# Performance work log

Hardware: AMD Instinct MI355X
Metric: run time of the kernel (lower is better)

The kernel has to match this reference:

```python
import jax, jax.numpy as jnp
import numpy as np

B, N, E = 4, 10000, 160000
IN, OUT, H, ED = 64, 128, 2, 1
SLOPE = 0.2  # GATv2Conv default negative_slope


def _seg_softmax(logits, seg, n):
    # logits: [Ef, H]; softmax over edges sharing the same dst node, per head
    m = jax.ops.segment_max(logits, seg, num_segments=n)
    e = jnp.exp(logits - m[seg])
    d = jax.ops.segment_sum(e, seg, num_segments=n)
    return e / d[seg]


def setup_inputs() -> dict:
    key = jax.random.key(0)
    ks = jax.random.split(key, 10)
    s = 0.05
    return {
        "node_feats": jax.random.normal(ks[0], (B, N, IN), jnp.float32),
        "edge_index": jax.random.randint(ks[1], (2, E), 0, N, dtype=jnp.int64),
        "edge_attr": jax.random.normal(ks[2], (E, ED), jnp.float32),
        "Wl": jax.random.normal(ks[3], (IN, H * OUT), jnp.float32) * s,
        "bl": jax.random.normal(ks[4], (H * OUT,), jnp.float32) * s,
        "Wr": jax.random.normal(ks[5], (IN, H * OUT), jnp.float32) * s,
        "br": jax.random.normal(ks[6], (H * OUT,), jnp.float32) * s,
        "We": jax.random.normal(ks[7], (ED, H * OUT), jnp.float32) * s,
        "att": jax.random.normal(ks[8], (H, OUT), jnp.float32) * s,
        "bias": jax.random.normal(ks[9], (H * OUT,), jnp.float32) * s,
    }


def reference(node_feats, edge_index, edge_attr, Wl, bl, Wr, br, We, att, bias):
    src, dst = edge_index[0], edge_index[1]
    # PyG add_self_loops(fill_value='mean'): self-loop attr = mean of incoming edge attrs per node
    ones = jnp.ones((E,), edge_attr.dtype)
    deg = jax.ops.segment_sum(ones, dst, num_segments=N)
    loop_attr = jax.ops.segment_sum(edge_attr, dst, num_segments=N) / jnp.maximum(deg, 1.0)[:, None]
    sl = jnp.arange(N)
    src_f = jnp.concatenate([src, sl])           # [Ef] with Ef = E + N
    dst_f = jnp.concatenate([dst, sl])
    e_feat = (jnp.concatenate([edge_attr, loop_attr], axis=0) @ We).reshape(-1, H, OUT)  # [Ef,H,C]

    xl = (node_feats @ Wl + bl).reshape(B, N, H, OUT)  # lin_l(x)
    xr = (node_feats @ Wr + br).reshape(B, N, H, OUT)  # lin_r(x)

    # GATv2: score on leaky_relu(x_l[src] + x_r[dst] + lin_edge(e))
    msg = jax.nn.leaky_relu(xl[:, src_f] + xr[:, dst_f] + e_feat[None], SLOPE)  # [B,Ef,H,C]
    logits = jnp.einsum('behc,hc->beh', msg, att)                               # [B,Ef,H]
    alpha = jax.vmap(lambda l: _seg_softmax(l, dst_f, N))(logits)               # [B,Ef,H]

    weighted = alpha[..., None] * xl[:, src_f]                                  # [B,Ef,H,C]
    out = jax.vmap(lambda w: jax.ops.segment_sum(w, dst_f, num_segments=N))(weighted)  # [B,N,H,C]
    return out.reshape(B, N, H * OUT) + bias
```

## Files before the change

kernel.cpp:

```cpp
#include <hip/hip_runtime.h>
#include <hip/hip_bf16.h>

#define BQ 4
#define NN 10000
#define EE 160000
#define HC 256
#define SLOPEK 0.2f
#define CAPE 128

typedef __attribute__((ext_vector_type(8))) short bf16x8;
typedef __attribute__((ext_vector_type(4))) float f32x4;
typedef __attribute__((ext_vector_type(2))) float f32x2;

__device__ __forceinline__ unsigned short f2bf(float f) {
    unsigned int u = __float_as_uint(f);
    u = (u + 0x7FFFu + ((u >> 16) & 1u)) >> 16;
    return (unsigned short)u;
}
__device__ __forceinline__ f32x2 bf2(unsigned int u) {
    return (f32x2){__uint_as_float(u << 16), __uint_as_float(u & 0xFFFF0000u)};
}

__global__ __launch_bounds__(256) void k_wpack(
    const float* __restrict__ Wl, const float* __restrict__ bl,
    const float* __restrict__ Wr, const float* __restrict__ br,
    unsigned short* __restrict__ wp, float* __restrict__ bp,
    int* __restrict__ zbase)
{
    if (blockIdx.x >= 130) {
        const int i = (blockIdx.x - 130) * 256 + threadIdx.x;
        if (i < 2 * NN) zbase[i] = 0;
        return;
    }
    const int tid = blockIdx.x * 256 + threadIdx.x;
    if (tid < 32768) {
        const int j  = tid & 7;
        const int l  = (tid >> 3) & 63;
        const int s  = (tid >> 9) & 1;
        const int ct = tid >> 10;
        const int col = ct * 16 + (l & 15);
        const int kk  = s * 32 + ((l >> 4) << 3) + j;
        const float w = (col < 256) ? Wl[kk * 256 + col] : Wr[kk * 256 + (col - 256)];
        wp[tid] = f2bf(w);
    } else if (tid < 32768 + 512) {
        const int c = tid - 32768;
        bp[c] = (c < 256) ? bl[c] : br[c - 256];
    }
}

__global__ __launch_bounds__(256) void k_pre(
    const float* __restrict__ x, const unsigned short* __restrict__ wp,
    const float* __restrict__ bp,
    unsigned short* __restrict__ xl, unsigned short* __restrict__ xr,
    const int* __restrict__ ei, const float* __restrict__ ea,
    int* __restrict__ cnt, float* __restrict__ asum,
    int2* __restrict__ cmeta)
{
    if (blockIdx.x >= 625) {
        const int e = (blockIdx.x - 625) * 256 + threadIdx.x;
        const int   sn = ei[e];
        const int   d  = ei[EE + e];
        const float a  = ea[e];
        const int pos  = atomicAdd(&cnt[d], 1);
        atomicAdd(&asum[d], a);
        if (pos < CAPE - 1)
            cmeta[d * CAPE + pos] = make_int2(sn << 10, __float_as_int(a));
        return;
    }
    const int w = threadIdx.x >> 6, l = threadIdx.x & 63;
    const int row0 = blockIdx.x * 64 + w * 16;
    const int arow = row0 + (l & 15);
    const float* xp = x + (size_t)arow * 64 + ((l >> 4) << 3);

    bf16x8 a[2];
#pragma unroll
    for (int s = 0; s < 2; ++s) {
        const float4 lo = *reinterpret_cast<const float4*>(xp + s * 32);
        const float4 hi = *reinterpret_cast<const float4*>(xp + s * 32 + 4);
        union { bf16x8 v; unsigned short u[8]; } t;
        t.u[0] = f2bf(lo.x); t.u[1] = f2bf(lo.y); t.u[2] = f2bf(lo.z); t.u[3] = f2bf(lo.w);
        t.u[4] = f2bf(hi.x); t.u[5] = f2bf(hi.y); t.u[6] = f2bf(hi.z); t.u[7] = f2bf(hi.w);
        a[s] = t.v;
    }
    const int colb = l & 15;
    const int rsub = (l >> 4) << 2;

    for (int g = 0; g < 8; ++g) {
        f32x4 acc[4] = {{0.f,0.f,0.f,0.f},{0.f,0.f,0.f,0.f},
                        {0.f,0.f,0.f,0.f},{0.f,0.f,0.f,0.f}};
#pragma unroll
        for (int c = 0; c < 4; ++c) {
            const int ct = g * 4 + c;
            const bf16x8 b0 = *reinterpret_cast<const bf16x8*>(wp + (((ct * 2 + 0) * 64 + l) << 3));
            const bf16x8 b1 = *reinterpret_cast<const bf16x8*>(wp + (((ct * 2 + 1) * 64 + l) << 3));
            acc[c] = __builtin_amdgcn_mfma_f32_16x16x32_bf16(a[0], b0, acc[c], 0, 0, 0);
            acc[c] = __builtin_amdgcn_mfma_f32_16x16x32_bf16(a[1], b1, acc[c], 0, 0, 0);
        }
#pragma unroll
        for (int c = 0; c < 4; ++c) {
            const int col = (g * 4 + c) * 16 + colb;
            const float bv = bp[col];
#pragma unroll
            for (int r = 0; r < 4; ++r) {
                const int row = row0 + rsub + r;
                const int bb = (row >= 20000) ? (row >= 30000 ? 3 : 2)
                                              : (row >= 10000 ? 1 : 0);
                const int n = row - bb * NN;
                const unsigned short h = f2bf(acc[c][r] + bv);
                if (col < 256) xl[(((size_t)(n * 4 + bb)) << 8) + col] = h;
                else           xr[(((size_t)(n * 4 + bb)) << 8) + (col - 256)] = h;
            }
        }
    }
}

__global__ __launch_bounds__(256) void k_gat(
    const unsigned short* __restrict__ xl, const unsigned short* __restrict__ xr,
    const int* __restrict__ cnt, const float* __restrict__ asum,
    const int2* __restrict__ cmeta,
    const float* __restrict__ We, const float* __restrict__ att,
    const float* __restrict__ bias, float* __restrict__ outp)
{
    const int t  = threadIdx.x;
    const int wv = t >> 6, ln = t & 63;
    const int W  = blockIdx.x * 4 + wv;
    const int n  = W >> 1;
    const int bp = W & 1;
    const int b  = bp * 2 + (ln >> 5);
    const int ch0 = (ln & 31) * 8;

    int dg0 = cnt[n];
    if (dg0 > 63) dg0 = 63;
    const int dg = __builtin_amdgcn_readfirstlane(dg0);
    const int2 md0 = cmeta[n * CAPE + ln];
    int   ms = md0.x;
    float ma = __int_as_float(md0.y);
    if (ln == dg) {
        ms = n << 10;
        ma = asum[n] / fmaxf((float)dg, 1.0f);
    }
    const int ntot = dg + 1;

    f32x2 we2[4], at2[4], xr2[4], acc2[4];
    {
        const float4* Wp = reinterpret_cast<const float4*>(We + ch0);
        const float4* Ap = reinterpret_cast<const float4*>(att + ch0);
#pragma unroll
        for (int j = 0; j < 2; ++j) {
            const float4 w4 = Wp[j], a4 = Ap[j];
            we2[2*j+0] = (f32x2){w4.x, w4.y};
            we2[2*j+1] = (f32x2){w4.z, w4.w};
            at2[2*j+0] = (f32x2){a4.x, a4.y};
            at2[2*j+1] = (f32x2){a4.z, a4.w};
        }
        const uint4 r0 = *reinterpret_cast<const uint4*>(
            xr + ((size_t)n << 10) + (b << 8) + ch0);
        xr2[0] = bf2(r0.x); xr2[1] = bf2(r0.y); xr2[2] = bf2(r0.z); xr2[3] = bf2(r0.w);
    }
    const f32x2 km1 = {SLOPEK - 1.f, SLOPEK - 1.f};
    const f32x2 z2  = {0.f, 0.f};
#pragma unroll
    for (int k = 0; k < 4; ++k) acc2[k] = z2;
    float sh = 0.f;

    const unsigned short* __restrict__ xlp = xl + (b << 8) + ch0;

    uint4 A0, A1, A2, A3;
    float ea0, ea1, ea2, ea3;

#define LOADSLOT(S, IDX) do { \
        const int ii_ = (IDX); \
        const int ic_ = ii_ < dg ? ii_ : dg; \
        const int   s_ = __builtin_amdgcn_readlane(ms, ic_); \
        ea##S = __int_as_float(__builtin_amdgcn_readlane(__float_as_int(ma), ic_)); \
        A##S = *reinterpret_cast<const uint4*>(xlp + s_); \
    } while (0)

    auto edgeC = [&](const uint4& A, float a0) {
        f32x2 xv2[4];
        xv2[0] = bf2(A.x); xv2[1] = bf2(A.y); xv2[2] = bf2(A.z); xv2[3] = bf2(A.w);

        const f32x2 a02 = {a0, a0};
        f32x2 qa = z2, qb = z2;
#pragma unroll
        for (int j = 0; j < 4; ++j) {
            f32x2 s = xv2[j] + xr2[j];
            f32x2 v = __builtin_elementwise_fma(a02, we2[j], s);
            f32x2 vm = __builtin_elementwise_min(v, z2);
            v = __builtin_elementwise_fma(km1, vm, v);
            if (j & 1) qb = __builtin_elementwise_fma(v, at2[j], qb);
            else       qa = __builtin_elementwise_fma(v, at2[j], qa);
        }
        const f32x2 q2 = qa + qb;
        float p = q2.x + q2.y;
        p += __shfl_xor(p, 1);
        p += __shfl_xor(p, 2);
        p += __shfl_xor(p, 4);
        p += __shfl_xor(p, 8);
        const float e = __expf(p);
        sh += e;
        const f32x2 e2 = {e, e};
#pragma unroll
        for (int j = 0; j < 4; ++j)
            acc2[j] = __builtin_elementwise_fma(e2, xv2[j], acc2[j]);
    };

    LOADSLOT(0, 0);
    LOADSLOT(1, 1);
    LOADSLOT(2, 2);

    int i = 0;
    for (; i + 3 < ntot; i += 4) {
        LOADSLOT(3, i + 3); edgeC(A0, ea0);
        LOADSLOT(0, i + 4); edgeC(A1, ea1);
        LOADSLOT(1, i + 5); edgeC(A2, ea2);
        LOADSLOT(2, i + 6); edgeC(A3, ea3);
    }
    if (i     < ntot) edgeC(A0, ea0);
    if (i + 1 < ntot) edgeC(A1, ea1);
    if (i + 2 < ntot) edgeC(A2, ea2);
#undef LOADSLOT

    const float inv = 1.0f / sh;
    float* ob = outp + (((size_t)(b * NN + n)) << 8) + ch0;
    const float4* Bp = reinterpret_cast<const float4*>(bias + ch0);
#pragma unroll
    for (int j = 0; j < 2; ++j) {
        const float4 b4 = Bp[j];
        float4 o;
        o.x = fmaf(acc2[2*j+0].x, inv, b4.x);
        o.y = fmaf(acc2[2*j+0].y, inv, b4.y);
        o.z = fmaf(acc2[2*j+1].x, inv, b4.z);
        o.w = fmaf(acc2[2*j+1].y, inv, b4.w);
        reinterpret_cast<float4*>(ob)[j] = o;
    }
}

extern "C" void kernel_launch(void* const* d_in, const int* in_sizes, int n_in,
                              void* d_out, int out_size, void* d_ws, size_t ws_size,
                              hipStream_t stream)
{
    (void)in_sizes; (void)n_in; (void)out_size; (void)ws_size;
    const float* x    = (const float*)d_in[0];
    const int*   ei   = (const int*)d_in[1];
    const float* ea   = (const float*)d_in[2];
    const float* Wl   = (const float*)d_in[3];
    const float* bl   = (const float*)d_in[4];
    const float* Wr   = (const float*)d_in[5];
    const float* br   = (const float*)d_in[6];
    const float* We   = (const float*)d_in[7];
    const float* att  = (const float*)d_in[8];
    const float* bias = (const float*)d_in[9];
    float* outp = (float*)d_out;

    const size_t R = (size_t)BQ * NN;
    unsigned short* xl16 = (unsigned short*)d_ws;
    unsigned short* xr16 = xl16 + R * HC;
    int*   cnt   = (int*)(xr16 + R * HC);
    float* asum  = (float*)(cnt + NN);
    int2*  cmeta = (int2*)(asum + NN);
    unsigned short* wp = (unsigned short*)(cmeta + (size_t)NN * CAPE);
    float* bp    = (float*)(wp + 32768);

    k_wpack<<<130 + (2 * NN + 255) / 256, 256, 0, stream>>>(Wl, bl, Wr, br, wp, bp, cnt);
    k_pre  <<<1250, 256, 0, stream>>>(x, wp, bp, xl16, xr16,
                                      ei, ea, cnt, asum, cmeta);
    k_gat  <<<(2 * NN) / 4, 256, 0, stream>>>(xl16, xr16, cnt, asum, cmeta,
                                              We, att, bias, outp);
}
```

Before: 89.98 us.

## Stage projection outputs in LDS for coalesced stores; deepen gather prefetch to 8

The projection kernel now writes bf16 results into a shared-memory tile and then emits 16-byte coalesced row stores to xl/xr, replacing scattered 2-byte global stores. The gather loop in the attention kernel is widened from a 4-deep to an 8-deep rotating prefetch of neighbor rows, to hide more memory latency. The exchange is extra LDS use and two barriers per half in k_pre, plus more registers in k_gat, which may reduce occupancy.

```diff
diff --git a/kernel.cpp b/kernel.cpp
--- a/kernel.cpp
+++ b/kernel.cpp
@@ -56,6 +56,8 @@
     int* __restrict__ cnt, float* __restrict__ asum,
     int2* __restrict__ cmeta)
 {
+    __shared__ unsigned short st[64][264];
+
     if (blockIdx.x >= 625) {
         const int e = (blockIdx.x - 625) * 256 + threadIdx.x;
         const int   sn = ei[e];
@@ -67,7 +69,8 @@
             cmeta[d * CAPE + pos] = make_int2(sn << 10, __float_as_int(a));
         return;
     }
-    const int w = threadIdx.x >> 6, l = threadIdx.x & 63;
+    const int t = threadIdx.x;
+    const int w = t >> 6, l = t & 63;
     const int row0 = blockIdx.x * 64 + w * 16;
     const int arow = row0 + (l & 15);
     const float* xp = x + (size_t)arow * 64 + ((l >> 4) << 3);
@@ -77,40 +80,45 @@
     for (int s = 0; s < 2; ++s) {
         const float4 lo = *reinterpret_cast<const float4*>(xp + s * 32);
         const float4 hi = *reinterpret_cast<const float4*>(xp + s * 32 + 4);
-        union { bf16x8 v; unsigned short u[8]; } t;
-        t.u[0] = f2bf(lo.x); t.u[1] = f2bf(lo.y); t.u[2] = f2bf(lo.z); t.u[3] = f2bf(lo.w);
-        t.u[4] = f2bf(hi.x); t.u[5] = f2bf(hi.y); t.u[6] = f2bf(hi.z); t.u[7] = f2bf(hi.w);
-        a[s] = t.v;
+        union { bf16x8 v; unsigned short u[8]; } tt;
+        tt.u[0] = f2bf(lo.x); tt.u[1] = f2bf(lo.y); tt.u[2] = f2bf(lo.z); tt.u[3] = f2bf(lo.w);
+        tt.u[4] = f2bf(hi.x); tt.u[5] = f2bf(hi.y); tt.u[6] = f2bf(hi.z); tt.u[7] = f2bf(hi.w);
+        a[s] = tt.v;
     }
     const int colb = l & 15;
     const int rsub = (l >> 4) << 2;
 
-    for (int g = 0; g < 8; ++g) {
-        f32x4 acc[4] = {{0.f,0.f,0.f,0.f},{0.f,0.f,0.f,0.f},
-                        {0.f,0.f,0.f,0.f},{0.f,0.f,0.f,0.f}};
-#pragma unroll
-        for (int c = 0; c < 4; ++c) {
-            const int ct = g * 4 + c;
-            const bf16x8 b0 = *reinterpret_cast<const bf16x8*>(wp + (((ct * 2 + 0) * 64 + l) << 3));
-            const bf16x8 b1 = *reinterpret_cast<const bf16x8*>(wp + (((ct * 2 + 1) * 64 + l) << 3));
-            acc[c] = __builtin_amdgcn_mfma_f32_16x16x32_bf16(a[0], b0, acc[c], 0, 0, 0);
-            acc[c] = __builtin_amdgcn_mfma_f32_16x16x32_bf16(a[1], b1, acc[c], 0, 0, 0);
-        }
-#pragma unroll
-        for (int c = 0; c < 4; ++c) {
-            const int col = (g * 4 + c) * 16 + colb;
-            const float bv = bp[col];
-#pragma unroll
-            for (int r = 0; r < 4; ++r) {
-                const int row = row0 + rsub + r;
-                const int bb = (row >= 20000) ? (row >= 30000 ? 3 : 2)
-                                              : (row >= 10000 ? 1 : 0);
-                const int n = row - bb * NN;
-                const unsigned short h = f2bf(acc[c][r] + bv);
-                if (col < 256) xl[(((size_t)(n * 4 + bb)) << 8) + col] = h;
-                else           xr[(((size_t)(n * 4 + bb)) << 8) + (col - 256)] = h;
+    for (int h = 0; h < 2; ++h) {
+        for (int g4 = 0; g4 < 4; ++g4) {
+            f32x4 acc[4] = {{0.f,0.f,0.f,0.f},{0.f,0.f,0.f,0.f},
+                            {0.f,0.f,0.f,0.f},{0.f,0.f,0.f,0.f}};
+#pragma unroll
+            for (int c = 0; c < 4; ++c) {
+                const int ct = h * 16 + g4 * 4 + c;
+                const bf16x8 b0 = *reinterpret_cast<const bf16x8*>(wp + (((ct * 2 + 0) * 64 + l) << 3));
+                const bf16x8 b1 = *reinterpret_cast<const bf16x8*>(wp + (((ct * 2 + 1) * 64 + l) << 3));
+                acc[c] = __builtin_amdgcn_mfma_f32_16x16x32_bf16(a[0], b0, acc[c], 0, 0, 0);
+                acc[c] = __builtin_amdgcn_mfma_f32_16x16x32_bf16(a[1], b1, acc[c], 0, 0, 0);
             }
-        }
+#pragma unroll
+            for (int c = 0; c < 4; ++c) {
+                const int colh = (g4 * 4 + c) * 16 + colb;
+                const float bv = bp[h * 256 + colh];
+#pragma unroll
+                for (int r = 0; r < 4; ++r)
+                    st[w * 16 + rsub + r][colh] = f2bf(acc[c][r] + bv);
+            }
+        }
+        __syncthreads();
+        unsigned short* __restrict__ dstb = h ? xr : xl;
+        for (int rr = (t >> 5); rr < 64; rr += 8) {
+            const int row = blockIdx.x * 64 + rr;
+            const int bb = row / NN;
+            const int n = row - bb * NN;
+            const uint4 v = *reinterpret_cast<const uint4*>(&st[rr][(t & 31) * 8]);
+            *reinterpret_cast<uint4*>(dstb + (((size_t)(n * 4 + bb)) << 8) + (t & 31) * 8) = v;
+        }
+        __syncthreads();
     }
 }
 
@@ -165,8 +173,8 @@
 
     const unsigned short* __restrict__ xlp = xl + (b << 8) + ch0;
 
-    uint4 A0, A1, A2, A3;
-    float ea0, ea1, ea2, ea3;
+    uint4 A0, A1, A2, A3, A4, A5, A6, A7;
+    float ea0, ea1, ea2, ea3, ea4, ea5, ea6, ea7;
 
 #define LOADSLOT(S, IDX) do { \
         const int ii_ = (IDX); \
@@ -205,20 +213,27 @@
             acc2[j] = __builtin_elementwise_fma(e2, xv2[j], acc2[j]);
     };
 
-    LOADSLOT(0, 0);
-    LOADSLOT(1, 1);
-    LOADSLOT(2, 2);
+    LOADSLOT(0, 0); LOADSLOT(1, 1); LOADSLOT(2, 2); LOADSLOT(3, 3);
+    LOADSLOT(4, 4); LOADSLOT(5, 5); LOADSLOT(6, 6);
 
     int i = 0;
-    for (; i + 3 < ntot; i += 4) {
-        LOADSLOT(3, i + 3); edgeC(A0, ea0);
-        LOADSLOT(0, i + 4); edgeC(A1, ea1);
-        LOADSLOT(1, i + 5); edgeC(A2, ea2);
-        LOADSLOT(2, i + 6); edgeC(A3, ea3);
+    for (; i + 7 < ntot; i += 8) {
+        LOADSLOT(7, i + 7);  edgeC(A0, ea0);
+        LOADSLOT(0, i + 8);  edgeC(A1, ea1);
+        LOADSLOT(1, i + 9);  edgeC(A2, ea2);
+        LOADSLOT(2, i + 10); edgeC(A3, ea3);
+        LOADSLOT(3, i + 11); edgeC(A4, ea4);
+        LOADSLOT(4, i + 12); edgeC(A5, ea5);
+        LOADSLOT(5, i + 13); edgeC(A6, ea6);
+        LOADSLOT(6, i + 14); edgeC(A7, ea7);
     }
     if (i     < ntot) edgeC(A0, ea0);
     if (i + 1 < ntot) edgeC(A1, ea1);
     if (i + 2 < ntot) edgeC(A2, ea2);
+    if (i + 3 < ntot) edgeC(A3, ea3);
+    if (i + 4 < ntot) edgeC(A4, ea4);
+    if (i + 5 < ntot) edgeC(A5, ea5);
+    if (i + 6 < ntot) edgeC(A6, ea6);
 #undef LOADSLOT
 
     const float inv = 1.0f / sh;
```

New measurement: 91.21 us. About the same (+1.4%).
